# Optimization experiments

Measured on AMD Instinct MI355X. Metric: run time of the kernel, lower is better.

The kernel has to match this reference:

```python
import jax, jax.numpy as jnp
import numpy as np

N, E, IN_DIM, HID = 8192, 65536, 128, 64
BN_EPS = 1e-5


def setup_inputs() -> dict:
    key = jax.random.key(0)
    ks = jax.random.split(key, 16)
    inp = {
        'h': jax.random.normal(ks[0], (N, IN_DIM), dtype=jnp.float32),
        'src': jax.random.randint(ks[1], (E,), 0, N, dtype=jnp.int32),
        'dst': jax.random.randint(ks[2], (E,), 0, N, dtype=jnp.int32),
        'proj1_w': jax.random.normal(ks[3], (HID * HID, IN_DIM), dtype=jnp.float32) * 0.02,
        'proj1_b': jax.random.normal(ks[4], (HID * HID,), dtype=jnp.float32) * 0.02,
        'proj2_w': jax.random.normal(ks[5], (HID, IN_DIM), dtype=jnp.float32) * 0.02,
        'proj2_b': jax.random.normal(ks[6], (HID,), dtype=jnp.float32) * 0.02,
        'conv_w': jax.random.normal(ks[7], (1, 2, 3), dtype=jnp.float32) * 0.2,
        'conv_b': jax.random.normal(ks[8], (1,), dtype=jnp.float32) * 0.2,
        'ep2_w': jax.random.normal(ks[9], (HID, IN_DIM), dtype=jnp.float32) * 0.02,
        'ep2_b': jax.random.normal(ks[10], (HID,), dtype=jnp.float32) * 0.02,
        'ep3_w': jax.random.normal(ks[11], (HID, HID), dtype=jnp.float32) * 0.02,
        'ep3_b': jax.random.normal(ks[12], (HID,), dtype=jnp.float32) * 0.02,
        'bn_gamma': jnp.ones((HID,), dtype=jnp.float32),
        'bn_beta': jnp.zeros((HID,), dtype=jnp.float32),
        'bn_mean': jnp.zeros((HID,), dtype=jnp.float32),
        'bn_var': jnp.ones((HID,), dtype=jnp.float32),
    }
    return inp


def reference(h, src, dst, proj1_w, proj1_b, proj2_w, proj2_b, conv_w, conv_b,
              ep2_w, ep2_b, ep3_w, ep3_b, bn_gamma, bn_beta, bn_mean, bn_var):
    # ---- local edge path: cat(src,dst) -> Conv1d(2->1,k3,p1) -> Linear ----
    edge = jnp.stack([h[src], h[dst]], axis=1)  # [E, 2, in_dim]
    conv = jax.lax.conv_general_dilated(
        edge, conv_w, window_strides=(1,), padding=[(1, 1)],
        dimension_numbers=('NCW', 'OIW', 'NCW'))  # [E, 1, in_dim]
    conv = conv + conv_b[None, :, None]
    lr_e_local = jnp.squeeze(conv, axis=1) @ ep2_w.T + ep2_b  # [E, hid]

    # ---- global edge path (SDDMM form of the dense NxN*hid mm) ----
    # torch: mm.view(N,hid,N).permute(0,2,1)[src,dst] == A[src] @ p2[dst]
    A = (h @ proj1_w.T + proj1_b).reshape(-1, HID, HID)  # [N, hid, hid]
    p2 = h @ proj2_w.T + proj2_b                          # [N, hid]
    lr_e_global = jnp.einsum('ejd,ed->ej', A[src], p2[dst])  # [E, hid]
    lr_e_global = lr_e_global @ ep3_w.T + ep3_b

    e = lr_e_local + lr_e_global
    # BatchNorm1d in eval mode (running stats), then ReLU; dropout is a no-op in eval.
    e = (e - bn_mean) * jax.lax.rsqrt(bn_var + BN_EPS) * bn_gamma + bn_beta
    return jax.nn.relu(e)
```

## Files before the change

### kernel.cpp

```cpp
#include <hip/hip_runtime.h>
#include <stdint.h>

#define NN   8192
#define EE   65536
#define IND  128
#define HID  64
#define NB   4096
#define BCAP 64

typedef __attribute__((ext_vector_type(8))) short short8;
typedef __attribute__((ext_vector_type(4))) float f32x4;
typedef _Float16 h2 __attribute__((ext_vector_type(2)));

__device__ __forceinline__ unsigned short f2bf(float f) {
  unsigned int x = __float_as_uint(f);
  x += 0x7fffu + ((x >> 16) & 1u);
  return (unsigned short)(x >> 16);
}
__device__ __forceinline__ float bfs(unsigned short u) { return __uint_as_float(((unsigned)u) << 16); }
__device__ __forceinline__ unsigned short f2h(float v) {
  return __builtin_bit_cast(unsigned short, (_Float16)v);
}
__device__ __forceinline__ h2 uh2(unsigned u) { return __builtin_bit_cast(h2, u); }

#if defined(__has_builtin)
#if __has_builtin(__builtin_amdgcn_fdot2)
#define HAVE_FDOT2 1
#endif
#endif
#ifdef HAVE_FDOT2
__device__ __forceinline__ float DOT2(h2 a, h2 b, float c) { return __builtin_amdgcn_fdot2(a, b, c, false); }
#else
__device__ __forceinline__ float DOT2(h2 a, h2 b, float c) {
  return c + (float)a.x * (float)b.x + (float)a.y * (float)b.y;
}
#endif

#define RL(x, j) __builtin_amdgcn_readlane((x), (j))

#define GLOAD_LDS16(g, l) __builtin_amdgcn_global_load_lds( \
    (const __attribute__((address_space(1))) unsigned int*)(g), \
    (__attribute__((address_space(3))) unsigned int*)(l), 16, 0, 0)

__global__ __launch_bounds__(256) void k_prep(const float* __restrict__ h,
                                              const int* __restrict__ src,
                                              const int* __restrict__ dst,
                                              const float* __restrict__ proj1_w,
                                              const float* __restrict__ proj1_b,
                                              const float* __restrict__ ep3_w,
                                              const float* __restrict__ proj2_w,
                                              const float* __restrict__ ep2_w,
                                              const float* __restrict__ ep2_b,
                                              const float* __restrict__ conv_w,
                                              const float* __restrict__ conv_b,
                                              const float* __restrict__ ep3_b,
                                              const float* __restrict__ bn_g,
                                              const float* __restrict__ bn_b,
                                              const float* __restrict__ bn_m,
                                              const float* __restrict__ bn_v,
                                              unsigned short* __restrict__ h_bf,
                                              int* __restrict__ cnt,
                                              int2* __restrict__ bucket,
                                              unsigned short* __restrict__ Wp_bf,
                                              float* __restrict__ bp,
                                              unsigned short* __restrict__ Wn,
                                              float* __restrict__ consts) {
  __shared__ union {
    struct { float ep3t[64][65]; float Ps[64][128]; float p1bs[64]; } w;
    float red[256];
  } sm;
  const int b = blockIdx.x;
  const int t = threadIdx.x;
  if (b < 512) {
    const int idx = b * 256 + t;
    const float4* s = (const float4*)h + (size_t)idx * 2;
    float4 a = s[0], bb = s[1];
    uint4 p;
    p.x = (unsigned)f2bf(a.x) | ((unsigned)f2bf(a.y) << 16);
    p.y = (unsigned)f2bf(a.z) | ((unsigned)f2bf(a.w) << 16);
    p.z = (unsigned)f2bf(bb.x) | ((unsigned)f2bf(bb.y) << 16);
    p.w = (unsigned)f2bf(bb.z) | ((unsigned)f2bf(bb.w) << 16);
    *(uint4*)(h_bf + (size_t)idx * 8) = p;
  } else if (b < 768) {
    const int e = (b - 512) * 256 + t;
    const int s = src[e], d = dst[e];
    const int p = atomicAdd(&cnt[s], 1);
    if (p < BCAP) bucket[(size_t)s * BCAP + p] = make_int2(e, d);
  } else if (b < 832) {
    const int d = b - 768;
#pragma unroll
    for (int s = 0; s < 16; ++s) {
      int idx = s * 256 + t;
      sm.w.ep3t[idx & 63][idx >> 6] = ep3_w[idx];
    }
#pragma unroll
    for (int s = 0; s < 8; ++s) {
      int idx = s * 256 + t;
      int j = idx >> 5, kq = idx & 31;
      *(float4*)&sm.w.Ps[j][kq * 4] = *(const float4*)(proj1_w + (size_t)(j * 64 + d) * IND + kq * 4);
    }
    if (t < 64) sm.w.p1bs[t] = proj1_b[t * 64 + d];
    __syncthreads();
    const int i = t & 63, kq = t >> 6;
    float acc[32];
#pragma unroll
    for (int kk = 0; kk < 32; ++kk) acc[kk] = 0.f;
    for (int j = 0; j < 64; ++j) {
      float e = sm.w.ep3t[j][i];
#pragma unroll
      for (int k4 = 0; k4 < 8; ++k4) {
        float4 pv = *(const float4*)&sm.w.Ps[j][kq * 32 + k4 * 4];
        acc[k4 * 4 + 0] += e * pv.x; acc[k4 * 4 + 1] += e * pv.y;
        acc[k4 * 4 + 2] += e * pv.z; acc[k4 * 4 + 3] += e * pv.w;
      }
    }
    unsigned short* dstp = Wp_bf + (size_t)(i * 64 + d) * IND + kq * 32;
#pragma unroll
    for (int kk = 0; kk < 32; kk += 2) {
      unsigned int p = (unsigned)f2bf(acc[kk]) | ((unsigned)f2bf(acc[kk + 1]) << 16);
      *(unsigned int*)(dstp + kk) = p;
    }
    if (kq == 0) {
      float bsum = 0.f;
      for (int j = 0; j < 64; ++j) bsum += sm.w.ep3t[j][i] * sm.w.p1bs[j];
      bp[i * 64 + d] = bsum;
    }
  } else {
    const int i = b - 832;
    const int x = t & 127;
    float u = 0.f, v = 0.f;
    for (int k = 0; k < 3; ++k) {
      int w = x + 1 - k;
      if (w >= 0 && w < IND) {
        float e = ep2_w[i * IND + w];
        u += conv_w[k] * e;
        v += conv_w[3 + k] * e;
      }
    }
    Wn[(size_t)i * IND + x]         = f2bf(proj2_w[i * IND + x]);
    Wn[(size_t)(64 + i) * IND + x]  = f2bf(u);
    Wn[(size_t)(128 + i) * IND + x] = f2bf(v);
    sm.red[t] = ep2_w[i * IND + x];
    __syncthreads();
    for (int s = 128; s > 0; s >>= 1) {
      if (t < s) sm.red[t] += sm.red[t + s];
      __syncthreads();
    }
    if (t == 0) {
      float scale = bn_g[i] * rsqrtf(bn_v[i] + 1e-5f);
      float shift = bn_b[i] - bn_m[i] * scale;
      float cb = conv_b[0] * sm.red[0] * 0.5f + ep2_b[i] + ep3_b[i];
      consts[i] = scale;
      consts[64 + i] = shift;
      consts[128 + i] = cb;
    }
  }
}

__global__ __launch_bounds__(256) void k_mm(const unsigned short* __restrict__ hbf,
                                            const unsigned short* __restrict__ Wbf,
                                            const float* __restrict__ bp,
                                            const unsigned short* __restrict__ Wn,
                                            const float* __restrict__ proj2_b,
                                            unsigned short* __restrict__ Bm,
                                            unsigned short* __restrict__ p2h,
                                            unsigned short* __restrict__ Ls,
                                            unsigned short* __restrict__ Ld) {
  __shared__ unsigned char sm[65536];
  const int t = threadIdx.x;
  if (blockIdx.x < 2048) {
    unsigned char* smA = sm;
    unsigned char* smB = sm + 32768;
    const int n0 = (blockIdx.x & 31) * 128, m0 = (blockIdx.x >> 5) * 128;
    const unsigned short* gA = hbf + (size_t)m0 * IND;
    const unsigned short* gB = Wbf + (size_t)n0 * IND;
#pragma unroll
    for (int s = 0; s < 8; ++s) {
      int p = s * 256 + t;
      int gp = (p & ~15) | ((p ^ (p >> 4)) & 15);
      GLOAD_LDS16(gA + gp * 8, smA + p * 16);
      GLOAD_LDS16(gB + gp * 8, smB + p * 16);
    }
    __syncthreads();
    const int w = t >> 6, lane = t & 63;
    const int wr = w >> 1, wc = w & 1;
    const int lrow = lane & 15, quad = lane >> 4;
    f32x4 acc[4][4] = {};
#pragma unroll
    for (int ks = 0; ks < 4; ++ks) {
      short8 af[4], bfr[4];
#pragma unroll
      for (int a = 0; a < 4; ++a) {
        int row = wr * 64 + a * 16 + lrow;
        int chunk = (ks * 4 + quad) ^ (row & 15);
        af[a] = *(const short8*)(smA + row * 256 + chunk * 16);
      }
#pragma unroll
      for (int b = 0; b < 4; ++b) {
        int row = wc * 64 + b * 16 + lrow;
        int chunk = (ks * 4 + quad) ^ (row & 15);
        bfr[b] = *(const short8*)(smB + row * 256 + chunk * 16);
      }
#pragma unroll
      for (int a = 0; a < 4; ++a)
#pragma unroll
        for (int b = 0; b < 4; ++b)
          acc[a][b] = __builtin_amdgcn_mfma_f32_16x16x32_bf16(af[a], bfr[b], acc[a][b], 0, 0, 0);
    }
    float bv[4];
#pragma unroll
    for (int b = 0; b < 4; ++b) bv[b] = bp[n0 + wc * 64 + b * 16 + lrow];
    __syncthreads();
#pragma unroll
    for (int a = 0; a < 4; ++a) {
      int R0 = wr * 64 + a * 16 + quad * 4;
#pragma unroll
      for (int b = 0; b < 4; ++b) {
        int C = wc * 64 + b * 16 + lrow;
#pragma unroll
        for (int v = 0; v < 4; ++v)
          *(unsigned short*)(sm + (size_t)(R0 + v) * 272 + C * 2) = f2h(acc[a][b][v] + bv[b]);
      }
    }
    __syncthreads();
#pragma unroll
    for (int s = 0; s < 8; ++s) {
      int p = s * 256 + t;
      int row = p >> 4, q = p & 15;
      uint4 val = *(const uint4*)(sm + (size_t)row * 272 + q * 16);
      *(uint4*)(Bm + (size_t)(m0 + row) * NB + n0 + q * 8) = val;
    }
  } else {
    unsigned char* smA = sm;
    unsigned char* smW = sm + 16384;
    const int m0 = (blockIdx.x - 2048) * 64;
#pragma unroll
    for (int s = 0; s < 4; ++s) {
      int p = s * 256 + t;
      int row = p >> 4, c = p & 15;
      int cs = c ^ (row & 15);
      GLOAD_LDS16(hbf + (size_t)(m0 + row) * IND + cs * 8, smA + p * 16);
    }
#pragma unroll
    for (int s = 0; s < 12; ++s) {
      int p = s * 256 + t;
      int row = p >> 4, c = p & 15;
      int cs = c ^ (row & 15);
      GLOAD_LDS16(Wn + (size_t)row * IND + cs * 8, smW + p * 16);
    }
    __syncthreads();
    const int w = t >> 6, lane = t & 63;
    const int lrow = lane & 15, quad = lane >> 4;
    f32x4 acc[12] = {};
#pragma unroll
    for (int ks = 0; ks < 4; ++ks) {
      const int chunk = (ks * 4 + quad) ^ lrow;
      short8 af = *(const short8*)(smA + (w * 16 + lrow) * 256 + chunk * 16);
#pragma unroll
      for (int n = 0; n < 12; ++n) {
        short8 bfr = *(const short8*)(smW + (n * 16 + lrow) * 256 + chunk * 16);
        acc[n] = __builtin_amdgcn_mfma_f32_16x16x32_bf16(af, bfr, acc[n], 0, 0, 0);
      }
    }
    const int row0 = m0 + w * 16 + quad * 4;
#pragma unroll
    for (int n = 0; n < 12; ++n) {
      int col = n * 16 + lrow;
      if (n < 4) {
        float b = proj2_b[col];
#pragma unroll
        for (int v = 0; v < 4; ++v)
          p2h[(size_t)(row0 + v) * HID + col] = f2h(acc[n][v] + b);
      } else if (n < 8) {
        int c2 = col - 64;
#pragma unroll
        for (int v = 0; v < 4; ++v)
          Ls[(size_t)(row0 + v) * HID + c2] = f2bf(acc[n][v]);
      } else {
        int c2 = col - 128;
#pragma unroll
        for (int v = 0; v < 4; ++v)
          Ld[(size_t)(row0 + v) * HID + c2] = f2bf(acc[n][v]);
      }
    }
  }
}

__global__ __launch_bounds__(256) void k_edge(const int* __restrict__ cnt,
                                              const int2* __restrict__ bucket,
                                              const unsigned short* __restrict__ Bm,
                                              const unsigned short* __restrict__ p2h,
                                              const unsigned short* __restrict__ Ls,
                                              const unsigned short* __restrict__ Ld,
                                              const float* __restrict__ consts,
                                              float* __restrict__ out) {
  const int t = threadIdx.x;
  const int w = t >> 6, lane = t & 63;
  const int s = blockIdx.x * 4 + w;
  const int n = min(cnt[s], BCAP);
  if (n == 0) return;
  const float sc = consts[lane], sh = consts[64 + lane];
  const float basev = bfs(Ls[(size_t)s * HID + lane]) + consts[128 + lane];
  const uint4* rowp = (const uint4*)(Bm + (size_t)s * NB) + lane * 8;
  uint4 r[8];
#pragma unroll
  for (int c = 0; c < 8; ++c) r[c] = rowp[c];
  const unsigned* p2u32 = (const unsigned*)p2h;
  const int lp = lane & 31;
  const int2 ed = (lane < n) ? bucket[(size_t)s * BCAP + lane] : make_int2(0, 0);
  int d = RL(ed.y, 0);
  unsigned p2u = p2u32[(size_t)d * 32 + lp];
  float ldv = bfs(Ld[(size_t)d * HID + lane]);
  for (int j = 0; j < n; ++j) {
    unsigned p2n = 0; float ldn = 0.f;
    if (j + 1 < n) {
      int dn = RL(ed.y, j + 1);
      p2n = p2u32[(size_t)dn * 32 + lp];
      ldn = bfs(Ld[(size_t)dn * HID + lane]);
    }
    float g0 = 0.f, g1 = 0.f, g2 = 0.f, g3 = 0.f;
#pragma unroll
    for (int c = 0; c < 8; ++c) {
      uint4 q = r[c];
      g0 = DOT2(uh2(q.x), uh2(RL(p2u, c * 4 + 0)), g0);
      g1 = DOT2(uh2(q.y), uh2(RL(p2u, c * 4 + 1)), g1);
      g2 = DOT2(uh2(q.z), uh2(RL(p2u, c * 4 + 2)), g2);
      g3 = DOT2(uh2(q.w), uh2(RL(p2u, c * 4 + 3)), g3);
    }
    const int e = RL(ed.x, j);
    float val = ((g0 + g1) + (g2 + g3)) + basev + ldv;
    val = val * sc + sh;
    out[(size_t)e * HID + lane] = fmaxf(val, 0.f);
    p2u = p2n; ldv = ldn;
  }
}

extern "C" void kernel_launch(void* const* d_in, const int* in_sizes, int n_in,
                              void* d_out, int out_size, void* d_ws, size_t ws_size,
                              hipStream_t stream) {
  const float* h       = (const float*)d_in[0];
  const int*   src     = (const int*)d_in[1];
  const int*   dst     = (const int*)d_in[2];
  const float* proj1_w = (const float*)d_in[3];
  const float* proj1_b = (const float*)d_in[4];
  const float* proj2_w = (const float*)d_in[5];
  const float* proj2_b = (const float*)d_in[6];
  const float* conv_w  = (const float*)d_in[7];
  const float* conv_b  = (const float*)d_in[8];
  const float* ep2_w   = (const float*)d_in[9];
  const float* ep2_b   = (const float*)d_in[10];
  const float* ep3_w   = (const float*)d_in[11];
  const float* ep3_b   = (const float*)d_in[12];
  const float* bn_g    = (const float*)d_in[13];
  const float* bn_b    = (const float*)d_in[14];
  const float* bn_m    = (const float*)d_in[15];
  const float* bn_v    = (const float*)d_in[16];

  char* ws = (char*)d_ws;
  unsigned short* Wp_bf = (unsigned short*)ws;  ws += (size_t)NB * IND * 2;
  unsigned short* h_bf  = (unsigned short*)ws;  ws += (size_t)NN * IND * 2;
  float* bp     = (float*)ws;                   ws += (size_t)NB * 4;
  unsigned short* Wn = (unsigned short*)ws;     ws += (size_t)192 * IND * 2;
  float* consts = (float*)ws;                   ws += 1024;
  int* cnt      = (int*)ws;                     ws += 8192 * 4;
  int2* bucket  = (int2*)ws;                    ws += (size_t)NN * BCAP * 8;
  unsigned short* p2h = (unsigned short*)ws;    ws += (size_t)NN * HID * 2;
  unsigned short* Ls = (unsigned short*)ws;     ws += (size_t)NN * HID * 2;
  unsigned short* Ld = (unsigned short*)ws;     ws += (size_t)NN * HID * 2;
  unsigned short* Bm = (unsigned short*)ws;

  hipMemsetAsync(cnt, 0, 8192 * sizeof(int), stream);
  k_prep<<<896, 256, 0, stream>>>(h, src, dst, proj1_w, proj1_b, ep3_w, proj2_w,
                                  ep2_w, ep2_b, conv_w, conv_b, ep3_b,
                                  bn_g, bn_b, bn_m, bn_v,
                                  h_bf, cnt, bucket, Wp_bf, bp, Wn, consts);
  k_mm<<<2176, 256, 0, stream>>>(h_bf, Wp_bf, bp, Wn, proj2_b, Bm, p2h, Ls, Ld);
  k_edge<<<NN / 4, 256, 0, stream>>>(cnt, bucket, Bm, p2h, Ls, Ld, consts, (float*)d_out);
}
```

Before: 165.6 us.

## Use MFMA for per-edge SDDMM and fold memset and bucketing into existing kernels

The per-edge contraction in k_edge changes from fdot2 with readlane broadcasts to 16x16x32 f16 MFMA tiles. Each wave handles 16 edges of a source node at once, and an identity-matrix MFMA adds the Ld term. p2 and Ld are packed into one 128-wide f16 row per node so one gather serves both, and Ls is kept in fp32. The cnt memset moves into k_prep and edge bucketing moves into k_mm, removing a separate memset launch and the serial dependency on bucketing. The trade-offs are wasted MFMA lanes for nodes with fewer than 16 edges, and an atomicAdd ordering change in the buckets that alters which edges are kept when a node exceeds BCAP.

```diff
diff --git a/kernel.cpp b/kernel.cpp
--- a/kernel.cpp
+++ b/kernel.cpp
@@ -10,41 +10,22 @@
 
 typedef __attribute__((ext_vector_type(8))) short short8;
 typedef __attribute__((ext_vector_type(4))) float f32x4;
-typedef _Float16 h2 __attribute__((ext_vector_type(2)));
+typedef _Float16 h8f __attribute__((ext_vector_type(8)));
 
 __device__ __forceinline__ unsigned short f2bf(float f) {
   unsigned int x = __float_as_uint(f);
   x += 0x7fffu + ((x >> 16) & 1u);
   return (unsigned short)(x >> 16);
 }
-__device__ __forceinline__ float bfs(unsigned short u) { return __uint_as_float(((unsigned)u) << 16); }
 __device__ __forceinline__ unsigned short f2h(float v) {
   return __builtin_bit_cast(unsigned short, (_Float16)v);
 }
-__device__ __forceinline__ h2 uh2(unsigned u) { return __builtin_bit_cast(h2, u); }
-
-#if defined(__has_builtin)
-#if __has_builtin(__builtin_amdgcn_fdot2)
-#define HAVE_FDOT2 1
-#endif
-#endif
-#ifdef HAVE_FDOT2
-__device__ __forceinline__ float DOT2(h2 a, h2 b, float c) { return __builtin_amdgcn_fdot2(a, b, c, false); }
-#else
-__device__ __forceinline__ float DOT2(h2 a, h2 b, float c) {
-  return c + (float)a.x * (float)b.x + (float)a.y * (float)b.y;
-}
-#endif
-
-#define RL(x, j) __builtin_amdgcn_readlane((x), (j))
 
 #define GLOAD_LDS16(g, l) __builtin_amdgcn_global_load_lds( \
     (const __attribute__((address_space(1))) unsigned int*)(g), \
     (__attribute__((address_space(3))) unsigned int*)(l), 16, 0, 0)
 
 __global__ __launch_bounds__(256) void k_prep(const float* __restrict__ h,
-                                              const int* __restrict__ src,
-                                              const int* __restrict__ dst,
                                               const float* __restrict__ proj1_w,
                                               const float* __restrict__ proj1_b,
                                               const float* __restrict__ ep3_w,
@@ -60,7 +41,6 @@
                                               const float* __restrict__ bn_v,
                                               unsigned short* __restrict__ h_bf,
                                               int* __restrict__ cnt,
-                                              int2* __restrict__ bucket,
                                               unsigned short* __restrict__ Wp_bf,
                                               float* __restrict__ bp,
                                               unsigned short* __restrict__ Wn,
@@ -72,6 +52,7 @@
   const int b = blockIdx.x;
   const int t = threadIdx.x;
   if (b < 512) {
+    if (b < 8) *(int4*)(cnt + (size_t)b * 1024 + t * 4) = make_int4(0, 0, 0, 0);
     const int idx = b * 256 + t;
     const float4* s = (const float4*)h + (size_t)idx * 2;
     float4 a = s[0], bb = s[1];
@@ -81,13 +62,8 @@
     p.z = (unsigned)f2bf(bb.x) | ((unsigned)f2bf(bb.y) << 16);
     p.w = (unsigned)f2bf(bb.z) | ((unsigned)f2bf(bb.w) << 16);
     *(uint4*)(h_bf + (size_t)idx * 8) = p;
-  } else if (b < 768) {
-    const int e = (b - 512) * 256 + t;
-    const int s = src[e], d = dst[e];
-    const int p = atomicAdd(&cnt[s], 1);
-    if (p < BCAP) bucket[(size_t)s * BCAP + p] = make_int2(e, d);
-  } else if (b < 832) {
-    const int d = b - 768;
+  } else if (b < 576) {
+    const int d = b - 512;
 #pragma unroll
     for (int s = 0; s < 16; ++s) {
       int idx = s * 256 + t;
@@ -126,7 +102,7 @@
       bp[i * 64 + d] = bsum;
     }
   } else {
-    const int i = b - 832;
+    const int i = b - 576;
     const int x = t & 127;
     float u = 0.f, v = 0.f;
     for (int k = 0; k < 3; ++k) {
@@ -162,10 +138,13 @@
                                             const float* __restrict__ bp,
                                             const unsigned short* __restrict__ Wn,
                                             const float* __restrict__ proj2_b,
+                                            const int* __restrict__ src,
+                                            const int* __restrict__ dst,
+                                            int* __restrict__ cnt,
+                                            int2* __restrict__ bucket,
                                             unsigned short* __restrict__ Bm,
-                                            unsigned short* __restrict__ p2h,
-                                            unsigned short* __restrict__ Ls,
-                                            unsigned short* __restrict__ Ld) {
+                                            unsigned short* __restrict__ pld,
+                                            float* __restrict__ Ls32) {
   __shared__ unsigned char sm[65536];
   const int t = threadIdx.x;
   if (blockIdx.x < 2048) {
@@ -230,7 +209,7 @@
       uint4 val = *(const uint4*)(sm + (size_t)row * 272 + q * 16);
       *(uint4*)(Bm + (size_t)(m0 + row) * NB + n0 + q * 8) = val;
     }
-  } else {
+  } else if (blockIdx.x < 2176) {
     unsigned char* smA = sm;
     unsigned char* smW = sm + 16384;
     const int m0 = (blockIdx.x - 2048) * 64;
@@ -270,28 +249,32 @@
         float b = proj2_b[col];
 #pragma unroll
         for (int v = 0; v < 4; ++v)
-          p2h[(size_t)(row0 + v) * HID + col] = f2h(acc[n][v] + b);
+          pld[(size_t)(row0 + v) * 128 + col] = f2h(acc[n][v] + b);
       } else if (n < 8) {
         int c2 = col - 64;
 #pragma unroll
         for (int v = 0; v < 4; ++v)
-          Ls[(size_t)(row0 + v) * HID + c2] = f2bf(acc[n][v]);
+          Ls32[(size_t)(row0 + v) * HID + c2] = acc[n][v];
       } else {
         int c2 = col - 128;
 #pragma unroll
         for (int v = 0; v < 4; ++v)
-          Ld[(size_t)(row0 + v) * HID + c2] = f2bf(acc[n][v]);
-      }
-    }
+          pld[(size_t)(row0 + v) * 128 + 64 + c2] = f2h(acc[n][v]);
+      }
+    }
+  } else {
+    const int e = (blockIdx.x - 2176) * 256 + t;
+    const int s = src[e], d = dst[e];
+    const int p = atomicAdd(&cnt[s], 1);
+    if (p < BCAP) bucket[(size_t)s * BCAP + p] = make_int2(e, d);
   }
 }
 
 __global__ __launch_bounds__(256) void k_edge(const int* __restrict__ cnt,
                                               const int2* __restrict__ bucket,
                                               const unsigned short* __restrict__ Bm,
-                                              const unsigned short* __restrict__ p2h,
-                                              const unsigned short* __restrict__ Ls,
-                                              const unsigned short* __restrict__ Ld,
+                                              const unsigned short* __restrict__ pld,
+                                              const float* __restrict__ Ls32,
                                               const float* __restrict__ consts,
                                               float* __restrict__ out) {
   const int t = threadIdx.x;
@@ -299,39 +282,64 @@
   const int s = blockIdx.x * 4 + w;
   const int n = min(cnt[s], BCAP);
   if (n == 0) return;
-  const float sc = consts[lane], sh = consts[64 + lane];
-  const float basev = bfs(Ls[(size_t)s * HID + lane]) + consts[128 + lane];
-  const uint4* rowp = (const uint4*)(Bm + (size_t)s * NB) + lane * 8;
-  uint4 r[8];
-#pragma unroll
-  for (int c = 0; c < 8; ++c) r[c] = rowp[c];
-  const unsigned* p2u32 = (const unsigned*)p2h;
-  const int lp = lane & 31;
-  const int2 ed = (lane < n) ? bucket[(size_t)s * BCAP + lane] : make_int2(0, 0);
-  int d = RL(ed.y, 0);
-  unsigned p2u = p2u32[(size_t)d * 32 + lp];
-  float ldv = bfs(Ld[(size_t)d * HID + lane]);
-  for (int j = 0; j < n; ++j) {
-    unsigned p2n = 0; float ldn = 0.f;
-    if (j + 1 < n) {
-      int dn = RL(ed.y, j + 1);
-      p2n = p2u32[(size_t)dn * 32 + lp];
-      ldn = bfs(Ld[(size_t)dn * HID + lane]);
-    }
-    float g0 = 0.f, g1 = 0.f, g2 = 0.f, g3 = 0.f;
-#pragma unroll
-    for (int c = 0; c < 8; ++c) {
-      uint4 q = r[c];
-      g0 = DOT2(uh2(q.x), uh2(RL(p2u, c * 4 + 0)), g0);
-      g1 = DOT2(uh2(q.y), uh2(RL(p2u, c * 4 + 1)), g1);
-      g2 = DOT2(uh2(q.z), uh2(RL(p2u, c * 4 + 2)), g2);
-      g3 = DOT2(uh2(q.w), uh2(RL(p2u, c * 4 + 3)), g3);
-    }
-    const int e = RL(ed.x, j);
-    float val = ((g0 + g1) + (g2 + g3)) + basev + ldv;
-    val = val * sc + sh;
-    out[(size_t)e * HID + lane] = fmaxf(val, 0.f);
-    p2u = p2n; ldv = ldn;
+  const int lrow = lane & 15, quad = lane >> 4;
+  const unsigned short* Brow = Bm + (size_t)s * NB;
+  h8f afr[4][2];
+#pragma unroll
+  for (int tt = 0; tt < 4; ++tt)
+#pragma unroll
+    for (int ks = 0; ks < 2; ++ks)
+      afr[tt][ks] = *(const h8f*)(Brow + (tt * 16 + lrow) * 64 + ks * 32 + quad * 8);
+  h8f idf[4];
+#pragma unroll
+  for (int tt = 0; tt < 4; ++tt) {
+    int j = tt * 16 + lrow - (tt >> 1) * 32 - quad * 8;
+    uint4 iw = make_uint4(0, 0, 0, 0);
+    if (j >= 0 && j < 8) {
+      unsigned val = 0x3C00u << ((j & 1) * 16);
+      int jw = j >> 1;
+      if (jw == 0) iw.x = val; else if (jw == 1) iw.y = val;
+      else if (jw == 2) iw.z = val; else iw.w = val;
+    }
+    idf[tt] = __builtin_bit_cast(h8f, iw);
+  }
+  float4 sc4[4], sh4[4], cbl[4];
+#pragma unroll
+  for (int tt = 0; tt < 4; ++tt) {
+    int ib = tt * 16 + quad * 4;
+    sc4[tt] = *(const float4*)(consts + ib);
+    sh4[tt] = *(const float4*)(consts + 64 + ib);
+    float4 cb = *(const float4*)(consts + 128 + ib);
+    float4 ls = *(const float4*)(Ls32 + (size_t)s * HID + ib);
+    cbl[tt] = make_float4(cb.x + ls.x, cb.y + ls.y, cb.z + ls.z, cb.w + ls.w);
+  }
+  for (int b0 = 0; b0 < n; b0 += 16) {
+    const int idx = b0 + lrow;
+    const int2 ed = bucket[(size_t)s * BCAP + min(idx, n - 1)];
+    const unsigned short* prow = pld + (size_t)ed.y * 128;
+    h8f bf0 = *(const h8f*)(prow + quad * 8);
+    h8f bf1 = *(const h8f*)(prow + 32 + quad * 8);
+    h8f bl0 = *(const h8f*)(prow + 64 + quad * 8);
+    h8f bl1 = *(const h8f*)(prow + 96 + quad * 8);
+    f32x4 acc[4] = {};
+#pragma unroll
+    for (int tt = 0; tt < 4; ++tt) {
+      acc[tt] = __builtin_amdgcn_mfma_f32_16x16x32_f16(afr[tt][0], bf0, acc[tt], 0, 0, 0);
+      acc[tt] = __builtin_amdgcn_mfma_f32_16x16x32_f16(afr[tt][1], bf1, acc[tt], 0, 0, 0);
+      acc[tt] = __builtin_amdgcn_mfma_f32_16x16x32_f16(idf[tt], (tt < 2) ? bl0 : bl1, acc[tt], 0, 0, 0);
+    }
+    if (idx < n) {
+      float* orow = out + (size_t)ed.x * HID;
+#pragma unroll
+      for (int tt = 0; tt < 4; ++tt) {
+        float4 o;
+        o.x = fmaxf((acc[tt][0] + cbl[tt].x) * sc4[tt].x + sh4[tt].x, 0.f);
+        o.y = fmaxf((acc[tt][1] + cbl[tt].y) * sc4[tt].y + sh4[tt].y, 0.f);
+        o.z = fmaxf((acc[tt][2] + cbl[tt].z) * sc4[tt].z + sh4[tt].z, 0.f);
+        o.w = fmaxf((acc[tt][3] + cbl[tt].w) * sc4[tt].w + sh4[tt].w, 0.f);
+        *(float4*)(orow + tt * 16 + quad * 4) = o;
+      }
+    }
   }
 }
 
@@ -364,16 +372,15 @@
   float* consts = (float*)ws;                   ws += 1024;
   int* cnt      = (int*)ws;                     ws += 8192 * 4;
   int2* bucket  = (int2*)ws;                    ws += (size_t)NN * BCAP * 8;
-  unsigned short* p2h = (unsigned short*)ws;    ws += (size_t)NN * HID * 2;
-  unsigned short* Ls = (unsigned short*)ws;     ws += (size_t)NN * HID * 2;
-  unsigned short* Ld = (unsigned short*)ws;     ws += (size_t)NN * HID * 2;
+  unsigned short* pld = (unsigned short*)ws;    ws += (size_t)NN * 128 * 2;
+  float* Ls32   = (float*)ws;                   ws += (size_t)NN * HID * 4;
   unsigned short* Bm = (unsigned short*)ws;
 
-  hipMemsetAsync(cnt, 0, 8192 * sizeof(int), stream);
-  k_prep<<<896, 256, 0, stream>>>(h, src, dst, proj1_w, proj1_b, ep3_w, proj2_w,
+  k_prep<<<640, 256, 0, stream>>>(h, proj1_w, proj1_b, ep3_w, proj2_w,
                                   ep2_w, ep2_b, conv_w, conv_b, ep3_b,
                                   bn_g, bn_b, bn_m, bn_v,
-                                  h_bf, cnt, bucket, Wp_bf, bp, Wn, consts);
-  k_mm<<<2176, 256, 0, stream>>>(h_bf, Wp_bf, bp, Wn, proj2_b, Bm, p2h, Ls, Ld);
-  k_edge<<<NN / 4, 256, 0, stream>>>(cnt, bucket, Bm, p2h, Ls, Ld, consts, (float*)d_out);
-}
+                                  h_bf, cnt, Wp_bf, bp, Wn, consts);
+  k_mm<<<2432, 256, 0, stream>>>(h_bf, Wp_bf, bp, Wn, proj2_b, src, dst,
+                                 cnt, bucket, Bm, pld, Ls32);
+  k_edge<<<NN / 4, 256, 0, stream>>>(cnt, bucket, Bm, pld, Ls32, consts, (float*)d_out);
+}
```

Measured after the change: 160.9 us. -2.9%, faster.
